# Kernel optimization log

Hardware: AMD Instinct MI355X
Metric: run time of the kernel (lower is better)

The kernel has to match this reference:

```python
import jax, jax.numpy as jnp
import numpy as np


def next_fast_len(n: int) -> int:
    # smallest m >= n whose only prime factors are 2, 3, 5 (matches torch ref)
    if n <= 2:
        return 2
    def is_fast(m):
        for p in (2, 3, 5):
            while m % p == 0:
                m //= p
        return m == 1
    while not is_fast(n):
        n += 1
    return n


def setup_inputs() -> dict:
    key = jax.random.key(0)
    k1, k2 = jax.random.split(key)
    B, C, H, W = 4, 64, 251, 509
    u = jax.random.normal(k1, (B, C, H, W), dtype=jnp.float32)
    k = jax.random.normal(k2, (B, C, H, W), dtype=jnp.float32)
    return {"u": u, "k": k}


def reference(u, k):
    # FFT-based 2D long convolution (FlashFFTConvInterface fallback path):
    # zero-pad to 2/3/5-smooth sizes, orthonormal rfft2, pointwise complex
    # multiply, irfft2, crop back, cast to input dtype.
    B, C, H, W = u.shape
    Hp, Wp = next_fast_len(H), next_fast_len(W)
    pad = ((0, 0), (0, 0), (0, Hp - H), (0, Wp - W))
    u_f = jnp.fft.rfft2(jnp.pad(u, pad).astype(jnp.float32), norm="ortho")
    k_f = jnp.fft.rfft2(jnp.pad(k, pad).astype(jnp.float32), norm="ortho")
    y = jnp.fft.irfft2(u_f * k_f, s=(Hp, Wp), norm="ortho")
    return y[..., :H, :W].astype(u.dtype)
```

## Files before the change

kernel.cpp:

```cpp
#include <hip/hip_runtime.h>
#include <math.h>


#define H_IN 251
#define W_IN 509
#define NIMG 256
#define LROW 518
#define CSTR 264

#define WBAR() __builtin_amdgcn_wave_barrier()

__device__ __forceinline__ float2 cadd(float2 a, float2 b){ return make_float2(a.x+b.x, a.y+b.y); }
__device__ __forceinline__ float2 csub(float2 a, float2 b){ return make_float2(a.x-b.x, a.y-b.y); }
__device__ __forceinline__ float2 cmul(float2 a, float2 b){ return make_float2(a.x*b.x-a.y*b.y, a.x*b.y+a.y*b.x); }
__device__ __forceinline__ float2 mnegi(float2 a){ return make_float2(a.y, -a.x); }

__device__ __forceinline__ void dft8(float2 x[8]) {
    const float s = 0.70710678118654752f;
    float2 y0=cadd(x[0],x[4]), y4=csub(x[0],x[4]);
    float2 y1=cadd(x[1],x[5]), y5=csub(x[1],x[5]);
    float2 y2=cadd(x[2],x[6]), y6=csub(x[2],x[6]);
    float2 y3=cadd(x[3],x[7]), y7=csub(x[3],x[7]);
    y5 = cmul(y5, make_float2(s, -s));
    y6 = mnegi(y6);
    y7 = cmul(y7, make_float2(-s, -s));
    float2 z0=cadd(y0,y2), z2=csub(y0,y2);
    float2 z1=cadd(y1,y3), z3=mnegi(csub(y1,y3));
    float2 z4=cadd(y4,y6), z6=csub(y4,y6);
    float2 z5=cadd(y5,y7), z7=mnegi(csub(y5,y7));
    float2 p0=cadd(z0,z1), p1=csub(z0,z1);
    float2 p2=cadd(z2,z3), p3=csub(z2,z3);
    float2 p4=cadd(z4,z5), p5=csub(z4,z5);
    float2 p6=cadd(z6,z7), p7=csub(z6,z7);
    x[0]=p0; x[1]=p4; x[2]=p2; x[3]=p6; x[4]=p1; x[5]=p5; x[6]=p3; x[7]=p7;
}

__device__ __forceinline__ void dft4(float2 x[4]) {
    float2 a=cadd(x[0],x[2]), c=csub(x[0],x[2]);
    float2 b=cadd(x[1],x[3]), d=mnegi(csub(x[1],x[3]));
    float2 p0=cadd(a,b), p1=csub(a,b);
    float2 p2=cadd(c,d), p3=csub(c,d);
    x[0]=p0; x[1]=p2; x[2]=p1; x[3]=p3;
}

__device__ __forceinline__ void tw8(float2 v[8], float ang1) {
    float sn, cs; __sincosf(ang1, &sn, &cs);
    const float2 w1 = make_float2(cs, sn);
    const float2 w2 = cmul(w1, w1);
    const float2 w3 = cmul(w2, w1);
    const float2 w4 = cmul(w2, w2);
    const float2 w5 = cmul(w4, w1);
    const float2 w6 = cmul(w4, w2);
    const float2 w7 = cmul(w4, w3);
    v[1] = cmul(v[1], w1); v[2] = cmul(v[2], w2); v[3] = cmul(v[3], w3);
    v[4] = cmul(v[4], w4); v[5] = cmul(v[5], w5); v[6] = cmul(v[6], w6);
    v[7] = cmul(v[7], w7);
}

__global__ __launch_bounds__(512, 4) void kA(const float* __restrict__ u,
                                             const float* __restrict__ kk,
                                             float2* __restrict__ zt,
                                             int img_base) {
    __shared__ float2 lds[8][LROW];
    const int imgl = blockIdx.x >> 5;
    const int h0   = (blockIdx.x & 31) << 3;
    const int rr   = threadIdx.x >> 6;
    const int t    = threadIdx.x & 63;
    const int h    = h0 + rr;
    const int img  = img_base + imgl;

    float2 X[8];
    {
        const size_t rowoff = ((size_t)img * H_IN + h) * W_IN;
        #pragma unroll
        for (int r = 0; r < 8; ++r) {
            const int w = t + (r << 6);
            float2 v = make_float2(0.f, 0.f);
            if (h < H_IN && w < W_IN) v = make_float2(u[rowoff + w], kk[rowoff + w]);
            X[r] = v;
        }
    }
    dft8(X);
    tw8(X, -6.2831853071795864f * (float)t / 512.0f);
    #pragma unroll
    for (int q = 0; q < 8; ++q) lds[rr][(q << 6) + (t ^ (q << 3))] = X[q];
    WBAR();

    const int q  = t >> 3;
    const int j1 = t & 7;
    float2 Y[8];
    #pragma unroll
    for (int j2 = 0; j2 < 8; ++j2)
        Y[j2] = lds[rr][(q << 6) + ((j1 + (j2 << 3)) ^ (q << 3))];
    dft8(Y);
    tw8(Y, -6.2831853071795864f * (float)j1 / 64.0f);
    WBAR();
    #pragma unroll
    for (int q2 = 0; q2 < 8; ++q2)
        lds[rr][((j1 << 6) + (q2 << 3) + q) ^ ((j1 & 1) << 3)] = Y[q2];
    WBAR();

    const int q2 = t & 7;
    float2 Z[8];
    #pragma unroll
    for (int j = 0; j < 8; ++j)
        Z[j] = lds[rr][((j << 6) + (q2 << 3) + q) ^ ((j & 1) << 3)];
    dft8(Z);
    WBAR();
    #pragma unroll
    for (int q3 = 0; q3 < 8; ++q3)
        lds[rr][((q3 << 6) + (q2 << 3) + q) ^ ((q3 & 1) << 3)] = Z[q3];
    __syncthreads();

    for (int idx = threadIdx.x; idx < 8 * 256; idx += 512) {
        const int w   = idx >> 2;
        const int hh2 = (idx & 3) << 1;
        const int wz  = w ^ (((w >> 6) & 1) << 3);
        const float2 a = lds[hh2][wz];
        const float2 b = lds[hh2 + 1][wz];
        reinterpret_cast<float4*>(zt)[((size_t)imgl * 512 + w) * 128 + ((h0 + hh2) >> 1)] =
            make_float4(a.x, a.y, b.x, b.y);
    }
}

__global__ __launch_bounds__(256, 6) void kB(float2* __restrict__ zt) {
    __shared__ float2 spec[8][CSTR];
    const int imgl = blockIdx.x / 65;
    const int bq   = blockIdx.x - imgl * 65;
    const int c    = threadIdx.x >> 5;
    const int t    = threadIdx.x & 31;
    const int pi   = c >> 1, side = c & 1;
    const int g    = (bq << 2) + pi;
    const bool valid = (g <= 256);
    const int w    = side ? ((512 - g) & 511) : g;
    const size_t colbase = ((size_t)imgl * 512 + w) * 256;

    float2 X[8];
    #pragma unroll
    for (int r = 0; r < 8; ++r) X[r] = zt[colbase + t + (r << 5)];

    const int q  = t >> 2;
    const int j1 = t & 3;
    const int rrq = t & 3;

    dft8(X);
    tw8(X, -6.2831853071795864f * (float)t / 256.0f);
    #pragma unroll
    for (int qq = 0; qq < 8; ++qq) spec[c][(qq << 5) + (t ^ ((qq & 3) << 3))] = X[qq];
    WBAR();

    float2 Y[8];
    #pragma unroll
    for (int j2 = 0; j2 < 8; ++j2)
        Y[j2] = spec[c][(q << 5) + ((j1 + (j2 << 2)) ^ ((q & 3) << 3))];
    dft8(Y);
    tw8(Y, -6.2831853071795864f * (float)j1 / 32.0f);
    WBAR();
    #pragma unroll
    for (int q2 = 0; q2 < 8; ++q2) spec[c][(j1 << 6) + (q2 << 3) + q] = Y[q2];
    WBAR();

    float2 Za[4], Zb[4];
    #pragma unroll
    for (int j = 0; j < 4; ++j) Za[j] = spec[c][(j << 6) + (rrq << 3) + q];
    #pragma unroll
    for (int j = 0; j < 4; ++j) Zb[j] = spec[c][(j << 6) + ((rrq + 4) << 3) + q];
    dft4(Za); dft4(Zb);
    WBAR();
    #pragma unroll
    for (int k = 0; k < 4; ++k) spec[c][(k << 6) + (rrq << 3) + q] = Za[k];
    #pragma unroll
    for (int k = 0; k < 4; ++k) spec[c][(k << 6) + ((rrq + 4) << 3) + q] = Zb[k];
    WBAR();

    {
        const int ti = threadIdx.x & 63;
        const int cA = (threadIdx.x >> 6) << 1;
        #pragma unroll
        for (int hi = 0; hi < 4; ++hi) {
            const int h  = ti + (hi << 6);
            const int hm = (256 - h) & 255;
            const float2 Zf = spec[cA][h];
            const float2 Zm = spec[cA + 1][hm];
            const float2 U = make_float2(0.5f * (Zf.x + Zm.x),  0.5f * (Zf.y - Zm.y));
            const float2 K = make_float2(0.5f * (Zf.y + Zm.y), -0.5f * (Zf.x - Zm.x));
            const float2 P = cmul(U, K);
            spec[cA][h]      = P;
            spec[cA + 1][hm] = make_float2(P.x, -P.y);
        }
    }
    WBAR();

    #pragma unroll
    for (int r = 0; r < 8; ++r) {
        float2 v = spec[c][t + (r << 5)];
        X[r] = make_float2(v.x, -v.y);
    }
    WBAR();
    dft8(X);
    tw8(X, -6.2831853071795864f * (float)t / 256.0f);
    #pragma unroll
    for (int qq = 0; qq < 8; ++qq) spec[c][(qq << 5) + (t ^ ((qq & 3) << 3))] = X[qq];
    WBAR();
    #pragma unroll
    for (int j2 = 0; j2 < 8; ++j2)
        Y[j2] = spec[c][(q << 5) + ((j1 + (j2 << 2)) ^ ((q & 3) << 3))];
    dft8(Y);
    tw8(Y, -6.2831853071795864f * (float)j1 / 32.0f);
    WBAR();
    #pragma unroll
    for (int q2 = 0; q2 < 8; ++q2) spec[c][(j1 << 6) + (q2 << 3) + q] = Y[q2];
    WBAR();
    #pragma unroll
    for (int j = 0; j < 4; ++j) Za[j] = spec[c][(j << 6) + (rrq << 3) + q];
    #pragma unroll
    for (int j = 0; j < 4; ++j) Zb[j] = spec[c][(j << 6) + ((rrq + 4) << 3) + q];
    dft4(Za); dft4(Zb);
    WBAR();
    #pragma unroll
    for (int k = 0; k < 4; ++k)
        spec[c][(k << 6) + (rrq << 3) + q] = make_float2(Za[k].x, -Za[k].y);
    #pragma unroll
    for (int k = 0; k < 4; ++k)
        spec[c][(k << 6) + ((rrq + 4) << 3) + q] = make_float2(Zb[k].x, -Zb[k].y);
    WBAR();

    if (valid && !side) {
        #pragma unroll
        for (int r = 0; r < 8; ++r) {
            const int h = t + (r << 5);
            zt[colbase + h] = spec[c][h];
        }
    }
}

__global__ __launch_bounds__(512, 4) void kC(const float2* __restrict__ zt,
                                             float* __restrict__ y,
                                             int img_base) {
    __shared__ float2 lds[8][LROW];
    const int imgl = blockIdx.x >> 5;
    const int h0   = (blockIdx.x & 31) << 3;
    const int rr   = threadIdx.x >> 6;
    const int t    = threadIdx.x & 63;
    const int img  = img_base + imgl;

    for (int idx = threadIdx.x; idx < 257 * 4; idx += 512) {
        const int w   = idx >> 2;
        const int hh2 = (idx & 3) << 1;
        const float4 v = reinterpret_cast<const float4*>(zt)
            [((size_t)imgl * 512 + w) * 128 + ((h0 + hh2) >> 1)];
        lds[hh2][w]     = make_float2(v.x, v.y);
        lds[hh2 + 1][w] = make_float2(v.z, v.w);
    }
    __syncthreads();

    for (int idx = threadIdx.x; idx < 255 * 8; idx += 512) {
        const int wp = 257 + (idx >> 3);
        const int hh = idx & 7;
        const float2 v = lds[hh][512 - wp];
        lds[hh][wp] = make_float2(v.x, -v.y);
    }
    __syncthreads();

    float2 X[8];
    #pragma unroll
    for (int r = 0; r < 8; ++r) {
        float2 v = lds[rr][t + (r << 6)];
        X[r] = make_float2(v.x, -v.y);
    }
    WBAR();

    dft8(X);
    tw8(X, -6.2831853071795864f * (float)t / 512.0f);
    #pragma unroll
    for (int q = 0; q < 8; ++q) lds[rr][(q << 6) + (t ^ (q << 3))] = X[q];
    WBAR();

    const int q  = t >> 3;
    const int j1 = t & 7;
    float2 Y[8];
    #pragma unroll
    for (int j2 = 0; j2 < 8; ++j2)
        Y[j2] = lds[rr][(q << 6) + ((j1 + (j2 << 3)) ^ (q << 3))];
    dft8(Y);
    tw8(Y, -6.2831853071795864f * (float)j1 / 64.0f);
    WBAR();
    #pragma unroll
    for (int q2 = 0; q2 < 8; ++q2)
        lds[rr][((j1 << 6) + (q2 << 3) + q) ^ ((j1 & 1) << 3)] = Y[q2];
    WBAR();

    const int q2 = t & 7;
    float2 Z[8];
    #pragma unroll
    for (int j = 0; j < 8; ++j)
        Z[j] = lds[rr][((j << 6) + (q2 << 3) + q) ^ ((j & 1) << 3)];
    dft8(Z);
    WBAR();
    #pragma unroll
    for (int q3 = 0; q3 < 8; ++q3)
        lds[rr][((q3 << 6) + (q2 << 3) + q) ^ ((q3 & 1) << 3)] = Z[q3];
    __syncthreads();

    const float scale = 2.1073424255447017e-08f;
    for (int idx = threadIdx.x; idx < 8 * 512; idx += 512) {
        const int w  = idx & 511;
        const int hh = idx >> 9;
        const int h  = h0 + hh;
        if (h < H_IN && w < W_IN)
            y[((size_t)img * H_IN + h) * W_IN + w] =
                lds[hh][w ^ (((w >> 6) & 1) << 3)].x * scale;
    }
}

extern "C" void kernel_launch(void* const* d_in, const int* in_sizes, int n_in,
                              void* d_out, int out_size, void* d_ws, size_t ws_size,
                              hipStream_t stream) {
    const float* u = (const float*)d_in[0];
    const float* k = (const float*)d_in[1];
    float* y = (float*)d_out;
    float2* zt = (float2*)d_ws;

    const size_t per_img = (size_t)512 * 256 * sizeof(float2);
    int chunk = (int)(ws_size / per_img);
    if (chunk > NIMG) chunk = NIMG;
    if (chunk < 1) chunk = 1;

    for (int base = 0; base < NIMG; base += chunk) {
        const int nimg = (NIMG - base < chunk) ? (NIMG - base) : chunk;
        kA<<<dim3(nimg * 32), dim3(512), 0, stream>>>(u, k, zt, base);
        kB<<<dim3(nimg * 65), dim3(256), 0, stream>>>(zt);
        kC<<<dim3(nimg * 32), dim3(512), 0, stream>>>(zt, y, base);
    }
}
```

Before: 523.4 us.

## Tile intermediate spectrum buffer by 8-row blocks for contiguous row-pass access

Changes the layout of the intermediate zt buffer from column-major (w-major, h contiguous) to a tiled layout where each 8-row block stores all 512 columns contiguously. The row kernels kA and kC now write and read one fully contiguous chunk per block instead of strided 16-byte pieces. The column kernel kB pays for this with strided gathers, 8 contiguous float2 per 4 KB-spaced group. It also trims the LDS row padding and unrolls the copy loops.

```diff
diff --git a/kernel.cpp b/kernel.cpp
--- a/kernel.cpp
+++ b/kernel.cpp
@@ -5,7 +5,7 @@
 #define H_IN 251
 #define W_IN 509
 #define NIMG 256
-#define LROW 518
+#define LROW 516
 #define CSTR 264
 
 #define WBAR() __builtin_amdgcn_wave_barrier()
@@ -63,7 +63,8 @@
                                              int img_base) {
     __shared__ float2 lds[8][LROW];
     const int imgl = blockIdx.x >> 5;
-    const int h0   = (blockIdx.x & 31) << 3;
+    const int h0b  = blockIdx.x & 31;
+    const int h0   = h0b << 3;
     const int rr   = threadIdx.x >> 6;
     const int t    = threadIdx.x & 63;
     const int h    = h0 + rr;
@@ -112,14 +113,19 @@
         lds[rr][((q3 << 6) + (q2 << 3) + q) ^ ((q3 & 1) << 3)] = Z[q3];
     __syncthreads();
 
-    for (int idx = threadIdx.x; idx < 8 * 256; idx += 512) {
-        const int w   = idx >> 2;
-        const int hh2 = (idx & 3) << 1;
-        const int wz  = w ^ (((w >> 6) & 1) << 3);
-        const float2 a = lds[hh2][wz];
-        const float2 b = lds[hh2 + 1][wz];
-        reinterpret_cast<float4*>(zt)[((size_t)imgl * 512 + w) * 128 + ((h0 + hh2) >> 1)] =
-            make_float4(a.x, a.y, b.x, b.y);
+    {
+        float4* __restrict__ zt4 = reinterpret_cast<float4*>(zt);
+        const size_t base4 = (((size_t)imgl << 5) + h0b) << 11;
+        #pragma unroll
+        for (int k = 0; k < 4; ++k) {
+            const int idx = (int)threadIdx.x + (k << 9);
+            const int w   = idx >> 2;
+            const int hh2 = (idx & 3) << 1;
+            const int wz  = w ^ (((w >> 6) & 1) << 3);
+            const float2 a = lds[hh2][wz];
+            const float2 b = lds[hh2 + 1][wz];
+            zt4[base4 + idx] = make_float4(a.x, a.y, b.x, b.y);
+        }
     }
 }
 
@@ -133,11 +139,12 @@
     const int g    = (bq << 2) + pi;
     const bool valid = (g <= 256);
     const int w    = side ? ((512 - g) & 511) : g;
-    const size_t colbase = ((size_t)imgl * 512 + w) * 256;
+    const size_t cb = ((size_t)imgl << 17) + ((size_t)(t >> 3) << 12)
+                    + ((size_t)w << 3) + (size_t)(t & 7);
 
     float2 X[8];
     #pragma unroll
-    for (int r = 0; r < 8; ++r) X[r] = zt[colbase + t + (r << 5)];
+    for (int r = 0; r < 8; ++r) X[r] = zt[cb + ((size_t)r << 14)];
 
     const int q  = t >> 2;
     const int j1 = t & 3;
@@ -227,10 +234,8 @@
 
     if (valid && !side) {
         #pragma unroll
-        for (int r = 0; r < 8; ++r) {
-            const int h = t + (r << 5);
-            zt[colbase + h] = spec[c][h];
-        }
+        for (int r = 0; r < 8; ++r)
+            zt[cb + ((size_t)r << 14)] = spec[c][t + (r << 5)];
     }
 }
 
@@ -239,18 +244,31 @@
                                              int img_base) {
     __shared__ float2 lds[8][LROW];
     const int imgl = blockIdx.x >> 5;
-    const int h0   = (blockIdx.x & 31) << 3;
+    const int h0b  = blockIdx.x & 31;
+    const int h0   = h0b << 3;
     const int rr   = threadIdx.x >> 6;
     const int t    = threadIdx.x & 63;
     const int img  = img_base + imgl;
 
-    for (int idx = threadIdx.x; idx < 257 * 4; idx += 512) {
-        const int w   = idx >> 2;
-        const int hh2 = (idx & 3) << 1;
-        const float4 v = reinterpret_cast<const float4*>(zt)
-            [((size_t)imgl * 512 + w) * 128 + ((h0 + hh2) >> 1)];
-        lds[hh2][w]     = make_float2(v.x, v.y);
-        lds[hh2 + 1][w] = make_float2(v.z, v.w);
+    {
+        const float4* __restrict__ zt4 = reinterpret_cast<const float4*>(zt);
+        const size_t base4 = (((size_t)imgl << 5) + h0b) << 11;
+        #pragma unroll
+        for (int k = 0; k < 2; ++k) {
+            const int idx = (int)threadIdx.x + (k << 9);
+            const int w   = idx >> 2;
+            const int hh2 = (idx & 3) << 1;
+            const float4 v = zt4[base4 + idx];
+            lds[hh2][w]     = make_float2(v.x, v.y);
+            lds[hh2 + 1][w] = make_float2(v.z, v.w);
+        }
+        if (threadIdx.x < 4) {
+            const int idx = 1024 + (int)threadIdx.x;
+            const int hh2 = (idx & 3) << 1;
+            const float4 v = zt4[base4 + idx];
+            lds[hh2][256]     = make_float2(v.x, v.y);
+            lds[hh2 + 1][256] = make_float2(v.z, v.w);
+        }
     }
     __syncthreads();
 
```

New measurement: 495.1 us. -5.4%, faster.
